# Kernel optimization log

Measured on AMD Instinct MI355X. Metric: run time of the kernel, lower is better.

The kernel has to match this reference:

```python
import jax, jax.numpy as jnp
import numpy as np

P = 5        # window_size
HEADS = 8
DH = 32      # dim_head
SCALE = DH ** -0.5


def setup_inputs() -> dict:
    key = jax.random.key(0)
    ks = jax.random.split(key, 5)
    b, c, h = 32, 256, 4000
    inner = HEADS * DH  # 256
    x = jax.random.normal(ks[0], (b, c, h), dtype=jnp.float32)
    W_qkv = jax.random.normal(ks[1], (c, inner * 3), dtype=jnp.float32) * (c ** -0.5)
    W_out = jax.random.normal(ks[2], (inner, c), dtype=jnp.float32) * (inner ** -0.5)
    b_out = jax.random.normal(ks[3], (c,), dtype=jnp.float32) * 0.02
    pos_embedding = jax.random.normal(ks[4], (2 * P - 1, 2 * P - 1), dtype=jnp.float32) * 0.02
    return {"x": x, "W_qkv": W_qkv, "W_out": W_out, "b_out": b_out, "pos_embedding": pos_embedding}


def _local_attn(x, W_qkv, W_out, b_out, pos_embedding):
    b, c, h = x.shape
    n = h // P
    # relative-position bias, faithful to torch indexing: rel_index[:,0]=(p-1-a), rel_index[:,1]=(p-a), shape (p,1)
    a = jnp.arange(P)
    bias = pos_embedding[(P - 1 - a)[:, None], (P - a)[:, None]]  # (p, 1)
    mask = jnp.zeros((P, P), x.dtype) + bias                      # (p, p)
    # 'b c (n p) -> (b n) p c'
    xw = x.reshape(b, c, n, P).transpose(0, 2, 3, 1).reshape(b * n, P, c)
    qkv = xw @ W_qkv  # (B, p, 3*inner)
    q, k, v = jnp.split(qkv, 3, axis=-1)
    split_heads = lambda t: t.reshape(b * n, P, HEADS, DH).transpose(0, 2, 1, 3)  # (B, h, p, d)
    q, k, v = split_heads(q), split_heads(k), split_heads(v)
    dots = jnp.einsum('bhid,bhjd->bhij', q, k) * SCALE + mask
    attn = jax.nn.softmax(dots, axis=-1)
    out = jnp.einsum('bhij,bhjd->bhid', attn, v)            # (B, h, p, d)
    out = out.transpose(0, 2, 1, 3).reshape(b * n, P, HEADS * DH)
    out = out @ W_out + b_out                                # (B, p, c_out)
    # '(b n) p c -> b c (n p)'
    out = out.reshape(b, n, P, -1).transpose(0, 3, 1, 2).reshape(b, -1, n * P)
    return out, attn


def reference(x, W_qkv, W_out, b_out, pos_embedding):
    return _local_attn(x, W_qkv, W_out, b_out, pos_embedding)
```

## Files before the change

### kernel.cpp

```cpp
#include <hip/hip_runtime.h>
#include <hip/hip_bf16.h>

typedef __attribute__((ext_vector_type(8))) short short8;
typedef __attribute__((ext_vector_type(4))) short short4v;
typedef __attribute__((ext_vector_type(4))) float f32x4;
typedef __attribute__((ext_vector_type(2))) float f32x2;

namespace {
constexpr int kC = 256;
constexpr int kH = 4000;
constexpr int kNW = 800;
constexpr int kP = 5;
constexpr float kScale = 0.17677669529663687f;
constexpr int kTotalWin = 25600;

constexpr int WPB = 6;
constexpr int ROWS = WPB * kP;
constexpr int NTHR = 512;

constexpr int WQKV_PACKED = 3 * 16 * 8 * 64 * 8;
constexpr int WOUT_PACKED = 16 * 8 * 64 * 8;

constexpr int RKOFF = 16384;
constexpr int SM_TOTAL = 32768;
}

__device__ inline unsigned short f2bs(float f) {
  __hip_bfloat16 h = __float2bfloat16(f);
  return *reinterpret_cast<unsigned short*>(&h);
}

__device__ inline f32x4 mfma16(short4v a, short4v b, f32x4 c) {
#if __has_builtin(__builtin_amdgcn_mfma_f32_16x16x16bf16_1k)
  return __builtin_amdgcn_mfma_f32_16x16x16bf16_1k(a, b, c, 0, 0, 0);
#elif __has_builtin(__builtin_amdgcn_mfma_f32_16x16x16_bf16)
  return __builtin_amdgcn_mfma_f32_16x16x16_bf16(a, b, c, 0, 0, 0);
#else
  f32x4 d;
  asm("v_mfma_f32_16x16x16_bf16 %0, %1, %2, %3"
      : "=v"(d)
      : "v"(a), "v"(b), "v"(c));
  return d;
#endif
}

__global__ void prep_weights(const float* __restrict__ Wqkv,
                             const float* __restrict__ Wout,
                             __hip_bfloat16* __restrict__ wq_p,
                             __hip_bfloat16* __restrict__ wo_p) {
  int idx = blockIdx.x * 256 + threadIdx.x;
  if (idx < WQKV_PACKED) {
    int i = idx & 7;
    int l = (idx >> 3) & 63;
    int kt = (idx >> 9) & 7;
    int nt = (idx >> 12) & 15;
    int part = idx >> 16;
    int k = kt * 32 + (l >> 4) * 8 + i;
    int col = part * 256 + nt * 16 + (l & 15);
    wq_p[idx] = __float2bfloat16(Wqkv[k * 768 + col]);
  }
  if (idx < WOUT_PACKED) {
    int i = idx & 7;
    int l = (idx >> 3) & 63;
    int kt = (idx >> 9) & 7;
    int nt = (idx >> 12) & 15;
    int k = kt * 32 + (l >> 4) * 8 + i;
    int col = nt * 16 + (l & 15);
    wo_p[idx] = __float2bfloat16(Wout[k * 256 + col]);
  }
}

__global__ __launch_bounds__(NTHR, 3) void local_attn_kernel(
    const float* __restrict__ x, const short* __restrict__ wq_p,
    const short* __restrict__ wo_p, const float* __restrict__ b_out,
    float* __restrict__ g_out, float* __restrict__ g_attn) {
  __shared__ __align__(16) char smem[SM_TOTAL];

  const int tid = threadIdx.x;
  const int lane = tid & 63;
  const int wid = tid >> 6;
  const int g = lane >> 4;
  const int l15 = lane & 15;

  const int widx0 = blockIdx.x * WPB;
  const int nwin = min(WPB, kTotalWin - widx0);
  const int nrows = nwin * kP;

#pragma unroll
  for (int pass = 0; pass < 8; ++pass) {
    int idx = pass * NTHR + tid;
    int cp = idx >> 5, hh = idx & 31;
    unsigned u = 0u;
    if (hh < nrows) {
      int wl = hh / kP, il = hh - wl * kP;
      int gw = widx0 + wl;
      int bb = gw / kNW;
      int hl = (gw - bb * kNW) * kP + il;
      const float* p = x + ((size_t)bb * kC + 2 * cp) * kH + hl;
      u = (unsigned)f2bs(p[0]) | ((unsigned)f2bs(p[kH]) << 16);
    }
    *(unsigned*)(smem + hh * 512 + ((cp * 4) ^ ((hh & 7) << 4))) = u;
  }
  __syncthreads();

  f32x4 acc_v[2][2];
  {
    f32x4 acc[2][2];
#pragma unroll
    for (int m = 0; m < 2; ++m)
#pragma unroll
      for (int n = 0; n < 2; ++n) acc[m][n] = (f32x4){0.f, 0.f, 0.f, 0.f};
#pragma unroll
    for (int kt = 0; kt < 8; ++kt) {
      short8 a[2];
#pragma unroll
      for (int m = 0; m < 2; ++m) {
        int row = m * 16 + l15;
        int kb = kt * 64 + (g << 4);
        a[m] = *(const short8*)(smem + row * 512 + (kb ^ ((row & 7) << 4)));
      }
#pragma unroll
      for (int n = 0; n < 2; ++n) {
        short8 b = *(const short8*)(
            wq_p + ((((16 + wid * 2 + n) * 8 + kt) * 64 + lane) * 8));
#pragma unroll
        for (int m = 0; m < 2; ++m)
          acc[m][n] =
              __builtin_amdgcn_mfma_f32_16x16x32_bf16(a[m], b, acc[m][n], 0, 0, 0);
      }
    }
#pragma unroll
    for (int m = 0; m < 2; ++m)
#pragma unroll
      for (int n = 0; n < 2; ++n)
#pragma unroll
        for (int r = 0; r < 4; ++r) {
          int row = m * 16 + (g << 2) + r;
          if (row < ROWS) {
            int col = wid * 32 + n * 16 + l15;
            *(__hip_bfloat16*)(smem + RKOFF + row * 512 +
                               ((col * 2) ^ ((row & 7) << 4))) =
                __float2bfloat16(acc[m][n][r]);
          }
        }
#pragma unroll
    for (int m = 0; m < 2; ++m)
#pragma unroll
      for (int n = 0; n < 2; ++n) acc_v[m][n] = (f32x4){0.f, 0.f, 0.f, 0.f};
#pragma unroll
    for (int kt = 0; kt < 8; ++kt) {
      short8 a[2];
#pragma unroll
      for (int m = 0; m < 2; ++m) {
        int row = m * 16 + l15;
        int kb = kt * 64 + (g << 4);
        a[m] = *(const short8*)(smem + row * 512 + (kb ^ ((row & 7) << 4)));
      }
#pragma unroll
      for (int n = 0; n < 2; ++n) {
        short8 b = *(const short8*)(
            wq_p + ((((32 + wid * 2 + n) * 8 + kt) * 64 + lane) * 8));
#pragma unroll
        for (int m = 0; m < 2; ++m)
          acc_v[m][n] = __builtin_amdgcn_mfma_f32_16x16x32_bf16(a[m], b,
                                                                acc_v[m][n], 0, 0, 0);
      }
    }
  }
  {
    f32x4 accq[2][2];
#pragma unroll
    for (int m = 0; m < 2; ++m)
#pragma unroll
      for (int n = 0; n < 2; ++n) accq[m][n] = (f32x4){0.f, 0.f, 0.f, 0.f};
#pragma unroll
    for (int kt = 0; kt < 8; ++kt) {
      short8 a[2];
#pragma unroll
      for (int m = 0; m < 2; ++m) {
        int row = m * 16 + l15;
        int kb = kt * 64 + (g << 4);
        a[m] = *(const short8*)(smem + row * 512 + (kb ^ ((row & 7) << 4)));
      }
#pragma unroll
      for (int n = 0; n < 2; ++n) {
        short8 b = *(const short8*)(
            wq_p + ((((wid * 2 + n) * 8 + kt) * 64 + lane) * 8));
#pragma unroll
        for (int m = 0; m < 2; ++m)
          accq[m][n] =
              __builtin_amdgcn_mfma_f32_16x16x32_bf16(a[m], b, accq[m][n], 0, 0, 0);
      }
    }
    __syncthreads();
#pragma unroll
    for (int m = 0; m < 2; ++m)
#pragma unroll
      for (int n = 0; n < 2; ++n)
#pragma unroll
        for (int r = 0; r < 4; ++r) {
          int row = m * 16 + (g << 2) + r;
          if (row < ROWS) {
            int col = wid * 32 + n * 16 + l15;
            *(__hip_bfloat16*)(smem + row * 512 +
                               ((col * 2) ^ ((row & 7) << 4))) =
                __float2bfloat16(accq[m][n][r]);
          }
        }
  }
  __syncthreads();

  {
    short8 kfa[2], qfb[2];
    const int cb = wid * 64 + (g << 4);
#pragma unroll
    for (int t = 0; t < 2; ++t) {
      int row = t * 16 + l15;
      int sw = (row & 7) << 4;
      kfa[t] = *(const short8*)(smem + RKOFF + row * 512 + (cb ^ sw));
      qfb[t] = *(const short8*)(smem + row * 512 + (cb ^ sw));
    }
    f32x4 sacc[2][2];
#pragma unroll
    for (int mk = 0; mk < 2; ++mk)
#pragma unroll
      for (int nq = 0; nq < 2; ++nq)
        sacc[mk][nq] = __builtin_amdgcn_mfma_f32_16x16x32_bf16(
            kfa[mk], qfb[nq], (f32x4){0.f, 0.f, 0.f, 0.f}, 0, 0, 0);

    short4v pb[2][2];
#pragma unroll
    for (int nq = 0; nq < 2; ++nq) {
      int q_abs = nq * 16 + l15;
      int w = q_abs / kP;
      int lo = w * kP;
      float psum = 0.f;
#pragma unroll
      for (int mk = 0; mk < 2; ++mk)
#pragma unroll
        for (int r = 0; r < 4; ++r) {
          int k = mk * 16 + (g << 2) + r;
          bool in = (q_abs < ROWS) && (k >= lo) && (k < lo + kP);
          float e = in ? __expf(sacc[mk][nq][r] * kScale) : 0.f;
          sacc[mk][nq][r] = e;
          psum += e;
        }
      psum += __shfl_xor(psum, 16);
      psum += __shfl_xor(psum, 32);
      float inv = psum > 0.f ? 1.f / psum : 0.f;
#pragma unroll
      for (int mk = 0; mk < 2; ++mk) {
        short4v t4;
#pragma unroll
        for (int r = 0; r < 4; ++r) {
          float pv = sacc[mk][nq][r] * inv;
          sacc[mk][nq][r] = pv;
          t4[r] = (short)f2bs(pv);
        }
        pb[mk][nq] = t4;
      }
      if (q_abs < nrows) {
        float* ap = g_attn + (size_t)(widx0 + w) * 200 + wid * 25 +
                    (q_abs - lo) * 5 - lo;
#pragma unroll
        for (int mk = 0; mk < 2; ++mk)
#pragma unroll
          for (int r = 0; r < 4; ++r) {
            int k = mk * 16 + (g << 2) + r;
            if (k >= lo && k < lo + kP) ap[k] = sacc[mk][nq][r];
          }
      }
    }
    short4v av[2][2];
#pragma unroll
    for (int kb2 = 0; kb2 < 2; ++kb2)
#pragma unroll
      for (int mt = 0; mt < 2; ++mt) {
        short4v t4;
#pragma unroll
        for (int r = 0; r < 4; ++r) t4[r] = (short)f2bs(acc_v[kb2][mt][r]);
        av[kb2][mt] = t4;
      }
#pragma unroll
    for (int mt = 0; mt < 2; ++mt)
#pragma unroll
      for (int nq = 0; nq < 2; ++nq) {
        f32x4 o = mfma16(av[0][mt], pb[0][nq], (f32x4){0.f, 0.f, 0.f, 0.f});
        o = mfma16(av[1][mt], pb[1][nq], o);
        int q_abs = nq * 16 + l15;
        if (q_abs < ROWS) {
          short4v o4;
#pragma unroll
          for (int r = 0; r < 4; ++r) o4[r] = (short)f2bs(o[r]);
          int byte = (wid * 64 + mt * 32 + g * 8) ^ ((q_abs & 7) << 4);
          *(short4v*)(smem + q_abs * 512 + byte) = o4;
        }
      }
  }
  __syncthreads();

  f32x4 acc2[2][2];
#pragma unroll
  for (int m = 0; m < 2; ++m)
#pragma unroll
    for (int n = 0; n < 2; ++n) acc2[m][n] = (f32x4){0.f, 0.f, 0.f, 0.f};
#pragma unroll
  for (int kt = 0; kt < 8; ++kt) {
    short8 a[2];
#pragma unroll
    for (int m = 0; m < 2; ++m) {
      int row = m * 16 + l15;
      int kb = kt * 64 + (g << 4);
      a[m] = *(const short8*)(smem + row * 512 + (kb ^ ((row & 7) << 4)));
    }
#pragma unroll
    for (int n = 0; n < 2; ++n) {
      short8 b =
          *(const short8*)(wo_p + ((((wid * 2 + n) * 8 + kt) * 64 + lane) * 8));
#pragma unroll
      for (int m = 0; m < 2; ++m)
        acc2[m][n] =
            __builtin_amdgcn_mfma_f32_16x16x32_bf16(a[m], b, acc2[m][n], 0, 0, 0);
    }
  }
  {
    const int b0 = widx0 / kNW;
    const bool fast = (nrows == ROWS) && (b0 == (widx0 + WPB - 1) / kNW);
#pragma unroll
    for (int n = 0; n < 2; ++n) {
      int col = wid * 32 + n * 16 + l15;
      float bias = b_out[col];
      if (fast) {
        int h0 = (widx0 - b0 * kNW) * kP;
        float* op = g_out + ((size_t)b0 * kC + col) * kH + h0 + g * 4;
#pragma unroll
        for (int m = 0; m < 2; ++m) {
          f32x2 v01 = {acc2[m][n][0] + bias, acc2[m][n][1] + bias};
          *(f32x2*)(op + m * 16) = v01;
          if (m * 16 + (g << 2) + 2 < ROWS) {
            f32x2 v23 = {acc2[m][n][2] + bias, acc2[m][n][3] + bias};
            *(f32x2*)(op + m * 16 + 2) = v23;
          }
        }
      } else {
#pragma unroll
        for (int m = 0; m < 2; ++m)
#pragma unroll
          for (int r = 0; r < 4; ++r) {
            int row = m * 16 + (g << 2) + r;
            if (row < nrows) {
              int gw = widx0 + row / kP;
              int bb = gw / kNW;
              int hl = (gw - bb * kNW) * kP + row % kP;
              g_out[((size_t)bb * kC + col) * kH + hl] = acc2[m][n][r] + bias;
            }
          }
      }
    }
  }
}

extern "C" void kernel_launch(void* const* d_in, const int* in_sizes, int n_in,
                              void* d_out, int out_size, void* d_ws,
                              size_t ws_size, hipStream_t stream) {
  const float* x = (const float*)d_in[0];
  const float* Wqkv = (const float*)d_in[1];
  const float* Wout = (const float*)d_in[2];
  const float* bout = (const float*)d_in[3];

  short* wq_p = (short*)d_ws;
  short* wo_p = wq_p + WQKV_PACKED;

  prep_weights<<<WQKV_PACKED / 256, 256, 0, stream>>>(
      Wqkv, Wout, (__hip_bfloat16*)wq_p, (__hip_bfloat16*)wo_p);

  float* g_out = (float*)d_out;
  float* g_attn = g_out + (size_t)32 * kC * kH;

  int nblocks = (kTotalWin + WPB - 1) / WPB;
  local_attn_kernel<<<nblocks, NTHR, 0, stream>>>(x, wq_p, wo_p, bout, g_out,
                                                  g_attn);
}
```

Baseline: 202.9 us.

## Process twelve windows per block as two 30-row groups to reuse weight fragments

Doubles the windows per block from 6 to 12, laid out as two 32-slot groups of 30 rows each, so every weight fragment loaded from global memory feeds four M-tiles instead of two. The K and V projections are merged into one k-loop that shares the A-fragment loads. The attention stage now loops over the two groups. Shared memory doubles to 64 KB and the occupancy hint drops from 3 to 2 blocks per CU, which raises register pressure and lowers wave occupancy in exchange for better weight reuse.

```diff
diff --git a/kernel.cpp b/kernel.cpp
--- a/kernel.cpp
+++ b/kernel.cpp
@@ -14,15 +14,17 @@
 constexpr float kScale = 0.17677669529663687f;
 constexpr int kTotalWin = 25600;
 
-constexpr int WPB = 6;
-constexpr int ROWS = WPB * kP;
+constexpr int WPB = 12;
+constexpr int ROWS_G = 30;
+constexpr int NROWS = 60;
+constexpr int MT = 4;
 constexpr int NTHR = 512;
 
 constexpr int WQKV_PACKED = 3 * 16 * 8 * 64 * 8;
 constexpr int WOUT_PACKED = 16 * 8 * 64 * 8;
 
-constexpr int RKOFF = 16384;
-constexpr int SM_TOTAL = 32768;
+constexpr int RKOFF = 32768;
+constexpr int SM_TOTAL = 65536;
 }
 
 __device__ inline unsigned short f2bs(float f) {
@@ -70,7 +72,7 @@
   }
 }
 
-__global__ __launch_bounds__(NTHR, 3) void local_attn_kernel(
+__global__ __launch_bounds__(NTHR, 2) void local_attn_kernel(
     const float* __restrict__ x, const short* __restrict__ wq_p,
     const short* __restrict__ wo_p, const float* __restrict__ b_out,
     float* __restrict__ g_out, float* __restrict__ g_attn) {
@@ -87,71 +89,84 @@
   const int nrows = nwin * kP;
 
 #pragma unroll
-  for (int pass = 0; pass < 8; ++pass) {
+  for (int pass = 0; pass < 16; ++pass) {
     int idx = pass * NTHR + tid;
-    int cp = idx >> 5, hh = idx & 31;
+    int cp = idx >> 6, slot = idx & 63;
+    int lr = slot & 31;
+    int grow = (slot >> 5) * ROWS_G + lr;
     unsigned u = 0u;
-    if (hh < nrows) {
-      int wl = hh / kP, il = hh - wl * kP;
+    if (lr < ROWS_G && grow < nrows) {
+      int wl = grow / kP, il = grow - wl * kP;
       int gw = widx0 + wl;
       int bb = gw / kNW;
       int hl = (gw - bb * kNW) * kP + il;
       const float* p = x + ((size_t)bb * kC + 2 * cp) * kH + hl;
       u = (unsigned)f2bs(p[0]) | ((unsigned)f2bs(p[kH]) << 16);
     }
-    *(unsigned*)(smem + hh * 512 + ((cp * 4) ^ ((hh & 7) << 4))) = u;
+    *(unsigned*)(smem + slot * 512 + ((cp * 4) ^ ((slot & 7) << 4))) = u;
   }
   __syncthreads();
 
-  f32x4 acc_v[2][2];
+  f32x4 acc_v[MT][2];
   {
-    f32x4 acc[2][2];
-#pragma unroll
-    for (int m = 0; m < 2; ++m)
-#pragma unroll
-      for (int n = 0; n < 2; ++n) acc[m][n] = (f32x4){0.f, 0.f, 0.f, 0.f};
+    f32x4 acck[MT][2];
+#pragma unroll
+    for (int m = 0; m < MT; ++m)
+#pragma unroll
+      for (int n = 0; n < 2; ++n) {
+        acck[m][n] = (f32x4){0.f, 0.f, 0.f, 0.f};
+        acc_v[m][n] = (f32x4){0.f, 0.f, 0.f, 0.f};
+      }
 #pragma unroll
     for (int kt = 0; kt < 8; ++kt) {
-      short8 a[2];
-#pragma unroll
-      for (int m = 0; m < 2; ++m) {
+      short8 a[MT];
+#pragma unroll
+      for (int m = 0; m < MT; ++m) {
         int row = m * 16 + l15;
         int kb = kt * 64 + (g << 4);
         a[m] = *(const short8*)(smem + row * 512 + (kb ^ ((row & 7) << 4)));
       }
 #pragma unroll
       for (int n = 0; n < 2; ++n) {
-        short8 b = *(const short8*)(
+        short8 bk = *(const short8*)(
             wq_p + ((((16 + wid * 2 + n) * 8 + kt) * 64 + lane) * 8));
-#pragma unroll
-        for (int m = 0; m < 2; ++m)
-          acc[m][n] =
-              __builtin_amdgcn_mfma_f32_16x16x32_bf16(a[m], b, acc[m][n], 0, 0, 0);
-      }
-    }
-#pragma unroll
-    for (int m = 0; m < 2; ++m)
+        short8 bv = *(const short8*)(
+            wq_p + ((((32 + wid * 2 + n) * 8 + kt) * 64 + lane) * 8));
+#pragma unroll
+        for (int m = 0; m < MT; ++m) {
+          acck[m][n] =
+              __builtin_amdgcn_mfma_f32_16x16x32_bf16(a[m], bk, acck[m][n], 0, 0, 0);
+          acc_v[m][n] =
+              __builtin_amdgcn_mfma_f32_16x16x32_bf16(a[m], bv, acc_v[m][n], 0, 0, 0);
+        }
+      }
+    }
+#pragma unroll
+    for (int m = 0; m < MT; ++m)
 #pragma unroll
       for (int n = 0; n < 2; ++n)
 #pragma unroll
         for (int r = 0; r < 4; ++r) {
-          int row = m * 16 + (g << 2) + r;
-          if (row < ROWS) {
+          int slot = m * 16 + (g << 2) + r;
+          if ((slot & 31) < ROWS_G) {
             int col = wid * 32 + n * 16 + l15;
-            *(__hip_bfloat16*)(smem + RKOFF + row * 512 +
-                               ((col * 2) ^ ((row & 7) << 4))) =
-                __float2bfloat16(acc[m][n][r]);
-          }
-        }
-#pragma unroll
-    for (int m = 0; m < 2; ++m)
-#pragma unroll
-      for (int n = 0; n < 2; ++n) acc_v[m][n] = (f32x4){0.f, 0.f, 0.f, 0.f};
+            *(__hip_bfloat16*)(smem + RKOFF + slot * 512 +
+                               ((col * 2) ^ ((slot & 7) << 4))) =
+                __float2bfloat16(acck[m][n][r]);
+          }
+        }
+  }
+  {
+    f32x4 accq[MT][2];
+#pragma unroll
+    for (int m = 0; m < MT; ++m)
+#pragma unroll
+      for (int n = 0; n < 2; ++n) accq[m][n] = (f32x4){0.f, 0.f, 0.f, 0.f};
 #pragma unroll
     for (int kt = 0; kt < 8; ++kt) {
-      short8 a[2];
-#pragma unroll
-      for (int m = 0; m < 2; ++m) {
+      short8 a[MT];
+#pragma unroll
+      for (int m = 0; m < MT; ++m) {
         int row = m * 16 + l15;
         int kb = kt * 64 + (g << 4);
         a[m] = *(const short8*)(smem + row * 512 + (kb ^ ((row & 7) << 4)));
@@ -159,66 +174,42 @@
 #pragma unroll
       for (int n = 0; n < 2; ++n) {
         short8 b = *(const short8*)(
-            wq_p + ((((32 + wid * 2 + n) * 8 + kt) * 64 + lane) * 8));
-#pragma unroll
-        for (int m = 0; m < 2; ++m)
-          acc_v[m][n] = __builtin_amdgcn_mfma_f32_16x16x32_bf16(a[m], b,
-                                                                acc_v[m][n], 0, 0, 0);
-      }
-    }
-  }
-  {
-    f32x4 accq[2][2];
-#pragma unroll
-    for (int m = 0; m < 2; ++m)
-#pragma unroll
-      for (int n = 0; n < 2; ++n) accq[m][n] = (f32x4){0.f, 0.f, 0.f, 0.f};
-#pragma unroll
-    for (int kt = 0; kt < 8; ++kt) {
-      short8 a[2];
-#pragma unroll
-      for (int m = 0; m < 2; ++m) {
-        int row = m * 16 + l15;
-        int kb = kt * 64 + (g << 4);
-        a[m] = *(const short8*)(smem + row * 512 + (kb ^ ((row & 7) << 4)));
-      }
-#pragma unroll
-      for (int n = 0; n < 2; ++n) {
-        short8 b = *(const short8*)(
             wq_p + ((((wid * 2 + n) * 8 + kt) * 64 + lane) * 8));
 #pragma unroll
-        for (int m = 0; m < 2; ++m)
+        for (int m = 0; m < MT; ++m)
           accq[m][n] =
               __builtin_amdgcn_mfma_f32_16x16x32_bf16(a[m], b, accq[m][n], 0, 0, 0);
       }
     }
     __syncthreads();
 #pragma unroll
-    for (int m = 0; m < 2; ++m)
+    for (int m = 0; m < MT; ++m)
 #pragma unroll
       for (int n = 0; n < 2; ++n)
 #pragma unroll
         for (int r = 0; r < 4; ++r) {
-          int row = m * 16 + (g << 2) + r;
-          if (row < ROWS) {
+          int slot = m * 16 + (g << 2) + r;
+          if ((slot & 31) < ROWS_G) {
             int col = wid * 32 + n * 16 + l15;
-            *(__hip_bfloat16*)(smem + row * 512 +
-                               ((col * 2) ^ ((row & 7) << 4))) =
+            *(__hip_bfloat16*)(smem + slot * 512 +
+                               ((col * 2) ^ ((slot & 7) << 4))) =
                 __float2bfloat16(accq[m][n][r]);
           }
         }
   }
   __syncthreads();
 
-  {
+  const int cb = wid * 64 + (g << 4);
+#pragma unroll
+  for (int gi = 0; gi < 2; ++gi) {
+    const int nrows_g = max(0, min(ROWS_G, nrows - gi * ROWS_G));
     short8 kfa[2], qfb[2];
-    const int cb = wid * 64 + (g << 4);
 #pragma unroll
     for (int t = 0; t < 2; ++t) {
-      int row = t * 16 + l15;
-      int sw = (row & 7) << 4;
-      kfa[t] = *(const short8*)(smem + RKOFF + row * 512 + (cb ^ sw));
-      qfb[t] = *(const short8*)(smem + row * 512 + (cb ^ sw));
+      int slot = gi * 32 + t * 16 + l15;
+      int sw = (slot & 7) << 4;
+      kfa[t] = *(const short8*)(smem + RKOFF + slot * 512 + (cb ^ sw));
+      qfb[t] = *(const short8*)(smem + slot * 512 + (cb ^ sw));
     }
     f32x4 sacc[2][2];
 #pragma unroll
@@ -240,7 +231,7 @@
 #pragma unroll
         for (int r = 0; r < 4; ++r) {
           int k = mk * 16 + (g << 2) + r;
-          bool in = (q_abs < ROWS) && (k >= lo) && (k < lo + kP);
+          bool in = (q_abs < ROWS_G) && (k >= lo) && (k < lo + kP);
           float e = in ? __expf(sacc[mk][nq][r] * kScale) : 0.f;
           sacc[mk][nq][r] = e;
           psum += e;
@@ -259,8 +250,9 @@
         }
         pb[mk][nq] = t4;
       }
-      if (q_abs < nrows) {
-        float* ap = g_attn + (size_t)(widx0 + w) * 200 + wid * 25 +
+      if (q_abs < nrows_g) {
+        float* ap = g_attn +
+                    (size_t)(widx0 + gi * (ROWS_G / kP) + w) * 200 + wid * 25 +
                     (q_abs - lo) * 5 - lo;
 #pragma unroll
         for (int mk = 0; mk < 2; ++mk)
@@ -275,40 +267,42 @@
 #pragma unroll
     for (int kb2 = 0; kb2 < 2; ++kb2)
 #pragma unroll
-      for (int mt = 0; mt < 2; ++mt) {
+      for (int dt = 0; dt < 2; ++dt) {
         short4v t4;
 #pragma unroll
-        for (int r = 0; r < 4; ++r) t4[r] = (short)f2bs(acc_v[kb2][mt][r]);
-        av[kb2][mt] = t4;
-      }
-#pragma unroll
-    for (int mt = 0; mt < 2; ++mt)
+        for (int r = 0; r < 4; ++r)
+          t4[r] = (short)f2bs(acc_v[gi * 2 + kb2][dt][r]);
+        av[kb2][dt] = t4;
+      }
+#pragma unroll
+    for (int dt = 0; dt < 2; ++dt)
 #pragma unroll
       for (int nq = 0; nq < 2; ++nq) {
-        f32x4 o = mfma16(av[0][mt], pb[0][nq], (f32x4){0.f, 0.f, 0.f, 0.f});
-        o = mfma16(av[1][mt], pb[1][nq], o);
+        f32x4 o = mfma16(av[0][dt], pb[0][nq], (f32x4){0.f, 0.f, 0.f, 0.f});
+        o = mfma16(av[1][dt], pb[1][nq], o);
         int q_abs = nq * 16 + l15;
-        if (q_abs < ROWS) {
+        if (q_abs < ROWS_G) {
+          int slot = gi * 32 + q_abs;
           short4v o4;
 #pragma unroll
           for (int r = 0; r < 4; ++r) o4[r] = (short)f2bs(o[r]);
-          int byte = (wid * 64 + mt * 32 + g * 8) ^ ((q_abs & 7) << 4);
-          *(short4v*)(smem + q_abs * 512 + byte) = o4;
+          int byte = (wid * 64 + dt * 32 + g * 8) ^ ((slot & 7) << 4);
+          *(short4v*)(smem + slot * 512 + byte) = o4;
         }
       }
   }
   __syncthreads();
 
-  f32x4 acc2[2][2];
-#pragma unroll
-  for (int m = 0; m < 2; ++m)
+  f32x4 acc2[MT][2];
+#pragma unroll
+  for (int m = 0; m < MT; ++m)
 #pragma unroll
     for (int n = 0; n < 2; ++n) acc2[m][n] = (f32x4){0.f, 0.f, 0.f, 0.f};
 #pragma unroll
   for (int kt = 0; kt < 8; ++kt) {
-    short8 a[2];
-#pragma unroll
-    for (int m = 0; m < 2; ++m) {
+    short8 a[MT];
+#pragma unroll
+    for (int m = 0; m < MT; ++m) {
       int row = m * 16 + l15;
       int kb = kt * 64 + (g << 4);
       a[m] = *(const short8*)(smem + row * 512 + (kb ^ ((row & 7) << 4)));
@@ -318,40 +312,44 @@
       short8 b =
           *(const short8*)(wo_p + ((((wid * 2 + n) * 8 + kt) * 64 + lane) * 8));
 #pragma unroll
-      for (int m = 0; m < 2; ++m)
+      for (int m = 0; m < MT; ++m)
         acc2[m][n] =
             __builtin_amdgcn_mfma_f32_16x16x32_bf16(a[m], b, acc2[m][n], 0, 0, 0);
     }
   }
   {
     const int b0 = widx0 / kNW;
-    const bool fast = (nrows == ROWS) && (b0 == (widx0 + WPB - 1) / kNW);
+    const bool fast =
+        (nwin == WPB) && (b0 == (widx0 + WPB - 1) / kNW);
 #pragma unroll
     for (int n = 0; n < 2; ++n) {
       int col = wid * 32 + n * 16 + l15;
       float bias = b_out[col];
       if (fast) {
         int h0 = (widx0 - b0 * kNW) * kP;
-        float* op = g_out + ((size_t)b0 * kC + col) * kH + h0 + g * 4;
-#pragma unroll
-        for (int m = 0; m < 2; ++m) {
+        float* opb = g_out + ((size_t)b0 * kC + col) * kH + h0;
+#pragma unroll
+        for (int m = 0; m < MT; ++m) {
+          float* op = opb + (m >> 1) * ROWS_G + (m & 1) * 16 + (g << 2);
           f32x2 v01 = {acc2[m][n][0] + bias, acc2[m][n][1] + bias};
-          *(f32x2*)(op + m * 16) = v01;
-          if (m * 16 + (g << 2) + 2 < ROWS) {
+          *(f32x2*)op = v01;
+          if (!(m & 1) || g < 3) {
             f32x2 v23 = {acc2[m][n][2] + bias, acc2[m][n][3] + bias};
-            *(f32x2*)(op + m * 16 + 2) = v23;
+            *(f32x2*)(op + 2) = v23;
           }
         }
       } else {
 #pragma unroll
-        for (int m = 0; m < 2; ++m)
+        for (int m = 0; m < MT; ++m)
 #pragma unroll
           for (int r = 0; r < 4; ++r) {
-            int row = m * 16 + (g << 2) + r;
-            if (row < nrows) {
-              int gw = widx0 + row / kP;
+            int slot = m * 16 + (g << 2) + r;
+            int lr = slot & 31;
+            int grow = (slot >> 5) * ROWS_G + lr;
+            if (lr < ROWS_G && grow < nrows) {
+              int gw = widx0 + grow / kP;
               int bb = gw / kNW;
-              int hl = (gw - bb * kNW) * kP + row % kP;
+              int hl = (gw - bb * kNW) * kP + grow % kP;
               g_out[((size_t)bb * kC + col) * kH + hl] = acc2[m][n][r] + bias;
             }
           }
```

After: 250.5 us. +23.5%, slower.
